# Kernel tuning notes

Hardware: AMD Instinct MI355X
Metric: run time of the kernel (lower is better)

The kernel has to match this reference:

```python
import jax, jax.numpy as jnp
import numpy as np

D_MODEL = 1024
NUM_HEADS = 16
SEG = 512            # segment_size
DIL = 4              # dilation_rate
HEAD_DIM = D_MODEL // NUM_HEADS


def setup_inputs() -> dict:
    key = jax.random.key(0)
    ks = jax.random.split(key, 5)
    B, S = 4, 4096
    sc = D_MODEL ** -0.5  # keep projected activations O(1) so softmax is not saturated
    def w(k):
        return jax.random.normal(k, (D_MODEL, D_MODEL), jnp.float32) * sc
    z = jnp.zeros((D_MODEL,), jnp.float32)
    return {
        "x": jax.random.normal(ks[0], (B, S, D_MODEL), jnp.float32),
        "Wq": w(ks[1]), "bq": z,
        "Wk": w(ks[2]), "bk": z,
        "Wv": w(ks[3]), "bv": z,
        "Wo": w(ks[4]), "bo": z,
    }


def reference(x, Wq, bq, Wk, bk, Wv, bv, Wo, bo):
    B, S, D = x.shape
    H, hd, seg, r = NUM_HEADS, HEAD_DIM, SEG, DIL
    scaling = hd ** -0.5

    Q = x @ Wq + bq
    K = x @ Wk + bk
    V = x @ Wv + bv

    pad = (-S) % seg
    if pad:
        Q = jnp.pad(Q, ((0, 0), (0, pad), (0, 0)))
        K = jnp.pad(K, ((0, 0), (0, pad), (0, 0)))
        V = jnp.pad(V, ((0, 0), (0, pad), (0, 0)))
    n = (S + pad) // seg          # num_segments
    sd = seg // r                 # dilated positions per segment per head

    # [B, n, sd, r, H, hd]: position within segment = t*r + offset
    def split(t):
        return t.reshape(B, n, sd, r, H, hd)

    offs = jnp.arange(H) % r      # per-head dilation offset sj = j % r
    hidx = jnp.arange(H)
    # vectorized per-head dilated gather -> [B, n, sd, H, hd]
    Qs = split(Q)[:, :, :, offs, hidx, :]
    Ks = split(K)[:, :, :, offs, hidx, :]
    Vs = split(V)[:, :, :, offs, hidx, :]

    # diagonal q.k score per dilated position, softmax over the segment's dilated positions
    scores = jnp.einsum('bnshd,bnshd->bnsh', Qs, Ks) * scaling
    probs = jax.nn.softmax(scores, axis=2)
    attn = probs[..., None] * Vs  # [B, n, sd, H, hd]

    # scatter back to each head's dilated positions; other positions stay zero
    out = jnp.zeros((B, n, sd, r, H, hd), x.dtype)
    out = out.at[:, :, :, offs, hidx, :].set(attn)
    out = out.reshape(B, n * seg, D)[:, :S]
    return out @ Wo + bo
```

## Files before the change

kernel.cpp:

```cpp
#include <hip/hip_runtime.h>
#include <hip/hip_bf16.h>

typedef unsigned short u16;
typedef unsigned int u32;
typedef __attribute__((ext_vector_type(8))) __bf16 bf16x8;
typedef __attribute__((ext_vector_type(4))) float f32x4;

#define NB 4
#define SQ 4096
#define DM 1024
#define RPC 4096
#define S4 (4 * DM)

#define VMCNT(n) asm volatile("s_waitcnt vmcnt(" #n ")" ::: "memory")
#define LGKM0()  asm volatile("s_waitcnt lgkmcnt(0)" ::: "memory")
#define BARRIER() asm volatile("s_barrier" ::: "memory")

__device__ __forceinline__ u16 f2b(float f) {
  u32 u = __builtin_bit_cast(u32, f);
  u32 r = u + 0x7fffu + ((u >> 16) & 1u);
  return (u16)(r >> 16);
}
__device__ __forceinline__ u32 cvt2(float lo, float hi) {
  u16 a = __builtin_bit_cast(u16, __float2bfloat16(lo));
  u16 b = __builtin_bit_cast(u16, __float2bfloat16(hi));
  return (u32)a | ((u32)b << 16);
}
__device__ __forceinline__ float dot2(u32 q, u32 k) {
  float ql = __builtin_bit_cast(float, q << 16);
  float qh = __builtin_bit_cast(float, q & 0xffff0000u);
  float kl = __builtin_bit_cast(float, k << 16);
  float kh = __builtin_bit_cast(float, k & 0xffff0000u);
  return ql * kl + qh * kh;
}
__device__ __forceinline__ u32 mul2(u32 v, float p) {
  float lo = __builtin_bit_cast(float, v << 16) * p;
  float hi = __builtin_bit_cast(float, v & 0xffff0000u) * p;
  return (u32)f2b(lo) | ((u32)f2b(hi) << 16);
}
__device__ __forceinline__ void gll16(const void* g, void* l) {
  __builtin_amdgcn_global_load_lds(
      (const __attribute__((address_space(1))) void*)g,
      (__attribute__((address_space(3))) void*)l, 16, 0, 0);
}

__global__ __launch_bounds__(256) void trans_qkv(const float* __restrict__ Wq,
                                                 const float* __restrict__ Wk,
                                                 const float* __restrict__ Wv,
                                                 u16* __restrict__ WTp) {
  __shared__ float T[64][65];
  const int k0 = blockIdx.x * 64, j0 = blockIdx.y * 64, c = blockIdx.z;
  const int msel = j0 >> 8;
  const float* W = (msel == 0) ? Wq : ((msel == 1) ? Wk : Wv);
  const int slot = (j0 & 255) >> 6;
  const int colbase = (c + 4 * slot) * 64;
  const int tid = threadIdx.x;
  const int rr = tid >> 6, cc = tid & 63;
#pragma unroll
  for (int it = 0; it < 16; ++it) {
    const int kk = rr + it * 4;
    T[kk][cc] = W[(size_t)(k0 + kk) * 1024 + colbase + cc];
  }
  __syncthreads();
  const int k64 = k0 >> 6;
  const int u = cc >> 3, e = cc & 7;
#pragma unroll
  for (int it = 0; it < 16; ++it) {
    const int jj = rr + it * 4;
    const int j = j0 + jj;
    const int n0 = j / 192, nrow = j - n0 * 192;
    WTp[((size_t)((c * 4 + n0) * 16 + k64)) * 12288 + nrow * 64 + (((u ^ (nrow & 7))) << 3) + e] =
        f2b(T[cc][jj]);
  }
}

__global__ __launch_bounds__(256) void trans_wo(const float* __restrict__ Wo,
                                                u16* __restrict__ WoTp) {
  __shared__ float T[64][65];
  const int j0 = blockIdx.x * 64, e0 = blockIdx.y * 64, c = blockIdx.z;
  const int rowbase = c * 64 + (j0 >> 6) * 256;
  const int tid = threadIdx.x;
  const int rr = tid >> 6, cc = tid & 63;
#pragma unroll
  for (int it = 0; it < 16; ++it) {
    const int jj = rr + it * 4;
    T[jj][cc] = Wo[(size_t)(rowbase + jj) * 1024 + e0 + cc];
  }
  __syncthreads();
  const int k64 = j0 >> 6;
  const int u = cc >> 3, e = cc & 7;
#pragma unroll
  for (int it = 0; it < 16; ++it) {
    const int ee = rr + it * 4;
    const int n = e0 + ee;
    const int n0 = n >> 8, nrow = n & 255;
    WoTp[((size_t)((c * 4 + n0) * 4 + k64)) * 16384 + nrow * 64 + (((u ^ (nrow & 7))) << 3) + e] =
        f2b(T[cc][ee]);
  }
}

__global__ __launch_bounds__(256) void bias_pack(const float* __restrict__ bq,
                                                 const float* __restrict__ bk,
                                                 const float* __restrict__ bv,
                                                 float* __restrict__ biasp) {
  const int idx = blockIdx.x * 256 + threadIdx.x;
  if (idx >= 3072) return;
  const int c = idx / 768, j = idx % 768;
  const int msel = j >> 8, jj = j & 255;
  const int col = (c + 4 * (jj >> 6)) * 64 + (jj & 63);
  const float* bb = (msel == 0) ? bq : ((msel == 1) ? bk : bv);
  biasp[idx] = bb[col];
}

__global__ __launch_bounds__(512, 2) void gemm_qkv(const float* __restrict__ x,
                                                   const u16* __restrict__ WTp,
                                                   const float* __restrict__ biasp,
                                                   u16* __restrict__ QKV) {
  __shared__ __align__(16) u16 As[2][16384];
  __shared__ __align__(16) u16 Bs[2][12288];
  const int p = blockIdx.x;
  const int L = (p & 7) * 32 + (p >> 3);
  const int c = L >> 6, rem = L & 63;
  const int m0 = rem >> 2, n0 = rem & 3;
  const int tid = threadIdx.x;
  const int lane = tid & 63, w = tid >> 6;
  const int wm = w >> 1, wn = w & 1;
  const int l15 = lane & 15, l16 = lane >> 4;

  const int rbase = m0 * 256;
  const int b = rbase >> 10;
  const int sbase = ((rbase & 1023) << 2) + c;
  const float* xA = x + (size_t)(b * SQ + sbase) * DM;

  int awoff[4];
  const float* aptr[4];
#pragma unroll
  for (int j = 0; j < 4; ++j) {
    const int r = (tid >> 3) + 64 * j;
    awoff[j] = r * 64 + (((tid & 7) ^ (r & 7)) << 3);
    aptr[j] = xA + (size_t)r * S4 + (tid & 7) * 8;
  }
  const u16* Bsrc = WTp + (size_t)((c * 4 + n0) * 16) * 12288;

  f32x4 acc[4][6];
#pragma unroll
  for (int i = 0; i < 4; ++i)
#pragma unroll
    for (int j = 0; j < 6; ++j) acc[i][j] = (f32x4){0.f, 0.f, 0.f, 0.f};

  int aoff[2][4], boff[2][6];
#pragma unroll
  for (int kk = 0; kk < 2; ++kk) {
    const int unit = kk * 4 + l16;
#pragma unroll
    for (int mf = 0; mf < 4; ++mf) {
      const int r = wm * 64 + mf * 16 + l15;
      aoff[kk][mf] = r * 64 + ((unit ^ (r & 7)) << 3);
    }
#pragma unroll
    for (int nf = 0; nf < 6; ++nf) {
      const int r = wn * 96 + nf * 16 + l15;
      boff[kk][nf] = r * 64 + ((unit ^ (r & 7)) << 3);
    }
  }

  float4 av[8];

#define LOADA(kt)                                                          \
  {                                                                        \
    _Pragma("unroll") for (int j = 0; j < 4; ++j) {                        \
      const float* s = aptr[j] + (kt) * 64;                                \
      av[2 * j] = *reinterpret_cast<const float4*>(s);                     \
      av[2 * j + 1] = *reinterpret_cast<const float4*>(s + 4);             \
    }                                                                      \
  }
#define DSWRITE(buf)                                                       \
  {                                                                        \
    _Pragma("unroll") for (int j = 0; j < 4; ++j) {                        \
      uint4 pk;                                                            \
      pk.x = cvt2(av[2 * j].x, av[2 * j].y);                               \
      pk.y = cvt2(av[2 * j].z, av[2 * j].w);                               \
      pk.z = cvt2(av[2 * j + 1].x, av[2 * j + 1].y);                       \
      pk.w = cvt2(av[2 * j + 1].z, av[2 * j + 1].w);                       \
      *reinterpret_cast<uint4*>(&As[buf][awoff[j]]) = pk;                  \
    }                                                                      \
  }
#define ISSUE_B(kt, buf)                                                   \
  {                                                                        \
    _Pragma("unroll") for (int i = 0; i < 3; ++i)                          \
        gll16(Bsrc + (size_t)(kt) * 12288 + tid * 8 + i * 4096,            \
              (char*)&Bs[buf][0] + tid * 16 + i * 8192);                   \
  }

  LOADA(0);
  DSWRITE(0);
  LOADA(1);
  ISSUE_B(0, 0);
  ISSUE_B(1, 1);
  VMCNT(6);
  DSWRITE(1);
  LOADA(2);
  VMCNT(8);
  LGKM0();
  BARRIER();

#pragma unroll 1
  for (int t = 0; t < 16; ++t) {
    const u16* Ab = As[t & 1];
    const u16* Bb = Bs[t & 1];
#pragma unroll
    for (int kk = 0; kk < 2; ++kk) {
      bf16x8 af[4], bv[6];
#pragma unroll
      for (int mf = 0; mf < 4; ++mf) af[mf] = *reinterpret_cast<const bf16x8*>(Ab + aoff[kk][mf]);
#pragma unroll
      for (int nf = 0; nf < 6; ++nf) bv[nf] = *reinterpret_cast<const bf16x8*>(Bb + boff[kk][nf]);
      __builtin_amdgcn_s_setprio(1);
#pragma unroll
      for (int mf = 0; mf < 4; ++mf)
#pragma unroll
        for (int nf = 0; nf < 6; ++nf)
          acc[mf][nf] = __builtin_amdgcn_mfma_f32_16x16x32_bf16(af[mf], bv[nf], acc[mf][nf], 0, 0, 0);
      __builtin_amdgcn_s_setprio(0);
    }
    if (t == 15) break;
    BARRIER();
    if (t <= 13) {
      VMCNT(8);
      ISSUE_B(t + 2, t & 1);
      VMCNT(3);
      DSWRITE(t & 1);
      if (t <= 12) LOADA(t + 3);
    } else {
      VMCNT(0);
    }
    LGKM0();
    BARRIER();
  }

  u16* outc = QKV + (size_t)c * RPC * 768;
#pragma unroll
  for (int mf = 0; mf < 4; ++mf) {
#pragma unroll
    for (int nf = 0; nf < 6; ++nf) {
      const int gcol = n0 * 192 + wn * 96 + nf * 16 + l15;
      const float bias = biasp[c * 768 + gcol];
#pragma unroll
      for (int jj = 0; jj < 4; ++jj) {
        const int rowt = wm * 64 + mf * 16 + l16 * 4 + jj;
        outc[(size_t)(rbase + rowt) * 768 + gcol] = f2b(acc[mf][nf][jj] + bias);
      }
    }
  }
#undef LOADA
#undef DSWRITE
#undef ISSUE_B
}

__global__ __launch_bounds__(256) void attn_k(const u16* __restrict__ QKV,
                                              u16* __restrict__ attnYp) {
  __shared__ float sc[4][128];
  const int blk = blockIdx.x;
  const int c = blk >> 6, b = (blk >> 4) & 3, n = (blk >> 1) & 7, half = blk & 1;
  const int r0 = b * 1024 + n * 128;
  const int m0 = r0 >> 8;
  const int rb = r0 & 255;
  const u16* base = QKV + ((size_t)c * RPC + r0) * 768;
  const int tid = threadIdx.x;
#pragma unroll
  for (int it = 0; it < 2; ++it) {
    const int tt = tid + it * 256;
    const int t = tt & 127, slot = tt >> 7;
    const u16* q = base + (size_t)t * 768 + slot * 64;
    float s = 0.f;
#pragma unroll
    for (int dd = 0; dd < 8; ++dd) {
      uint4 qa = *reinterpret_cast<const uint4*>(q + dd * 8);
      uint4 ka = *reinterpret_cast<const uint4*>(q + 256 + dd * 8);
      s += dot2(qa.x, ka.x) + dot2(qa.y, ka.y) + dot2(qa.z, ka.z) + dot2(qa.w, ka.w);
    }
    sc[slot][t] = s * 0.125f;
  }
  __syncthreads();
  const int w = tid >> 6, lane = tid & 63;
  float v0 = sc[w][lane], v1 = sc[w][lane + 64];
  float m = fmaxf(v0, v1);
#pragma unroll
  for (int off = 32; off; off >>= 1) m = fmaxf(m, __shfl_xor(m, off));
  float e0 = __expf(v0 - m), e1 = __expf(v1 - m);
  float ssum = e0 + e1;
#pragma unroll
  for (int off = 32; off; off >>= 1) ssum += __shfl_xor(ssum, off);
  const float inv = 1.f / ssum;
  sc[w][lane] = e0 * inv;
  sc[w][lane + 64] = e1 * inv;
  __syncthreads();
  u16* yout = attnYp + (size_t)((c * 16 + m0) * 4) * 16384;
#pragma unroll
  for (int it = 0; it < 8; ++it) {
    const int vi = tid + it * 256;
    const int t = vi >> 4, c8 = (vi & 15) + half * 16;
    const float pr = sc[c8 >> 3][t];
    uint4 va = *reinterpret_cast<const uint4*>(base + (size_t)t * 768 + 512 + c8 * 8);
    uint4 ra;
    ra.x = mul2(va.x, pr); ra.y = mul2(va.y, pr); ra.z = mul2(va.z, pr); ra.w = mul2(va.w, pr);
    const int rloc = rb + t;
    const int k64 = c8 >> 3, uu = c8 & 7, pp = uu ^ (rloc & 7);
    *reinterpret_cast<uint4*>(yout + k64 * 16384 + rloc * 64 + pp * 8) = ra;
  }
}

__global__ __launch_bounds__(512, 2) void gemm_out(const u16* __restrict__ attnYp,
                                                   const u16* __restrict__ WoTp,
                                                   const float* __restrict__ bo,
                                                   float* __restrict__ out) {
  __shared__ __align__(16) u16 As[2][16384];
  __shared__ __align__(16) u16 Bs[2][16384];
  const int p = blockIdx.x;
  const int L = (p & 7) * 32 + (p >> 3);
  const int c = L >> 6, rem = L & 63;
  const int m0 = rem >> 2, n0 = rem & 3;
  const int tid = threadIdx.x;
  const int lane = tid & 63, w = tid >> 6;
  const int wm = w >> 1, wn = w & 1;
  const int l15 = lane & 15, l16 = lane >> 4;

  const u16* Asrc = attnYp + (size_t)((c * 16 + m0) * 4) * 16384;
  const u16* Bsrc = WoTp + (size_t)((c * 4 + n0) * 4) * 16384;

  f32x4 acc[4][8];
#pragma unroll
  for (int i = 0; i < 4; ++i)
#pragma unroll
    for (int j = 0; j < 8; ++j) acc[i][j] = (f32x4){0.f, 0.f, 0.f, 0.f};

  int aoff[2][4], boff[2][8];
#pragma unroll
  for (int kk = 0; kk < 2; ++kk) {
    const int unit = kk * 4 + l16;
#pragma unroll
    for (int mf = 0; mf < 4; ++mf) {
      const int r = wm * 64 + mf * 16 + l15;
      aoff[kk][mf] = r * 64 + ((unit ^ (r & 7)) << 3);
    }
#pragma unroll
    for (int nf = 0; nf < 8; ++nf) {
      const int r = wn * 128 + nf * 16 + l15;
      boff[kk][nf] = r * 64 + ((unit ^ (r & 7)) << 3);
    }
  }

#define ISSUE(kt, buf)                                                     \
  {                                                                        \
    _Pragma("unroll") for (int i = 0; i < 4; ++i) {                        \
      gll16(Asrc + (size_t)(kt) * 16384 + tid * 8 + i * 4096,              \
            (char*)&As[buf][0] + tid * 16 + i * 8192);                     \
      gll16(Bsrc + (size_t)(kt) * 16384 + tid * 8 + i * 4096,              \
            (char*)&Bs[buf][0] + tid * 16 + i * 8192);                     \
    }                                                                      \
  }

  ISSUE(0, 0);
  ISSUE(1, 1);
  VMCNT(8);
  BARRIER();

#pragma unroll 1
  for (int t = 0; t < 4; ++t) {
    const u16* Ab = As[t & 1];
    const u16* Bb = Bs[t & 1];
#pragma unroll
    for (int kk = 0; kk < 2; ++kk) {
      bf16x8 af[4], bv[8];
#pragma unroll
      for (int mf = 0; mf < 4; ++mf) af[mf] = *reinterpret_cast<const bf16x8*>(Ab + aoff[kk][mf]);
#pragma unroll
      for (int nf = 0; nf < 8; ++nf) bv[nf] = *reinterpret_cast<const bf16x8*>(Bb + boff[kk][nf]);
      __builtin_amdgcn_s_setprio(1);
#pragma unroll
      for (int mf = 0; mf < 4; ++mf)
#pragma unroll
        for (int nf = 0; nf < 8; ++nf)
          acc[mf][nf] = __builtin_amdgcn_mfma_f32_16x16x32_bf16(af[mf], bv[nf], acc[mf][nf], 0, 0, 0);
      __builtin_amdgcn_s_setprio(0);
    }
    if (t == 3) break;
    BARRIER();
    if (t <= 1) {
      ISSUE(t + 2, t & 1);
      VMCNT(8);
    } else {
      VMCNT(0);
    }
    BARRIER();
  }
#undef ISSUE

  const int rbase = m0 * 256;
  const int b = rbase >> 10;
  const int sbase = ((rbase & 1023) << 2) + c;
  float* outp = out + (size_t)(b * SQ + sbase) * DM;
#pragma unroll
  for (int mf = 0; mf < 4; ++mf) {
#pragma unroll
    for (int nf = 0; nf < 8; ++nf) {
      const int gcol = n0 * 256 + wn * 128 + nf * 16 + l15;
      const float bias = bo[gcol];
#pragma unroll
      for (int jj = 0; jj < 4; ++jj) {
        const int rowt = wm * 64 + mf * 16 + l16 * 4 + jj;
        outp[(size_t)rowt * S4 + gcol] = acc[mf][nf][jj] + bias;
      }
    }
  }
}

extern "C" void kernel_launch(void* const* d_in, const int* in_sizes, int n_in,
                              void* d_out, int out_size, void* d_ws, size_t ws_size,
                              hipStream_t stream) {
  const float* x  = (const float*)d_in[0];
  const float* Wq = (const float*)d_in[1];
  const float* bq = (const float*)d_in[2];
  const float* Wk = (const float*)d_in[3];
  const float* bk = (const float*)d_in[4];
  const float* Wv = (const float*)d_in[5];
  const float* bv = (const float*)d_in[6];
  const float* Wo = (const float*)d_in[7];
  const float* bo = (const float*)d_in[8];
  float* out = (float*)d_out;

  char* ws = (char*)d_ws;
  u16*   WTp   = (u16*)(ws);
  float* biasp = (float*)(ws + 6291456);
  u16*   WoTp  = (u16*)(ws + 6303744);
  u16*   QKV   = (u16*)(ws + 8400896);
  u16*   attnYp= (u16*)(ws + 33566720);

  trans_qkv<<<dim3(16, 12, 4), 256, 0, stream>>>(Wq, Wk, Wv, WTp);
  bias_pack<<<12, 256, 0, stream>>>(bq, bk, bv, biasp);
  trans_wo<<<dim3(4, 16, 4), 256, 0, stream>>>(Wo, WoTp);
  gemm_qkv<<<256, 512, 0, stream>>>(x, WTp, biasp, QKV);
  attn_k<<<256, 256, 0, stream>>>(QKV, attnYp);
  gemm_out<<<256, 512, 0, stream>>>(attnYp, WoTp, bo, out);
}
```

Before: 84.05 us.

## Triple-buffer B tiles and overlap A staging with MFMA in QKV GEMM

Restructures the QKV GEMM main loop into a two-step unrolled pipeline. B tiles now rotate through three LDS buffers, and A uses two register sets. A fragments are read into registers before a barrier, which lets the next A global load, the B async copy and the LDS write of the following A tile be interleaved with the MFMA clusters. This removes one barrier per iteration and the serialized wait between compute and staging. In exchange it uses more LDS (an extra B buffer) and more registers, which may reduce occupancy under the 2-blocks launch bound.

Result: slower. 129.8 us (+54.5%).

```diff
diff --git a/kernel.cpp b/kernel.cpp
--- a/kernel.cpp
+++ b/kernel.cpp
@@ -116,8 +116,8 @@
                                                    const u16* __restrict__ WTp,
                                                    const float* __restrict__ biasp,
                                                    u16* __restrict__ QKV) {
-  __shared__ __align__(16) u16 As[2][16384];
-  __shared__ __align__(16) u16 Bs[2][12288];
+  __shared__ __align__(16) u16 As2[2 * 16384];
+  __shared__ __align__(16) u16 Bs3[3 * 12288];
   const int p = blockIdx.x;
   const int L = (p & 7) * 32 + (p >> 3);
   const int c = L >> 6, rem = L & 63;
@@ -132,14 +132,8 @@
   const int sbase = ((rbase & 1023) << 2) + c;
   const float* xA = x + (size_t)(b * SQ + sbase) * DM;
 
-  int awoff[4];
-  const float* aptr[4];
-#pragma unroll
-  for (int j = 0; j < 4; ++j) {
-    const int r = (tid >> 3) + 64 * j;
-    awoff[j] = r * 64 + (((tid & 7) ^ (r & 7)) << 3);
-    aptr[j] = xA + (size_t)r * S4 + (tid & 7) * 8;
-  }
+  const int aw0 = ((tid >> 3) * 64) + ((((tid & 7) ^ ((tid >> 3) & 7))) << 3);
+  const float* aptr = xA + (size_t)(tid >> 3) * S4 + (tid & 7) * 8;
   const u16* Bsrc = WTp + (size_t)((c * 4 + n0) * 16) * 12288;
 
   f32x4 acc[4][6];
@@ -148,94 +142,111 @@
 #pragma unroll
     for (int j = 0; j < 6; ++j) acc[i][j] = (f32x4){0.f, 0.f, 0.f, 0.f};
 
-  int aoff[2][4], boff[2][6];
+  int abase[2], bbase[2];
 #pragma unroll
   for (int kk = 0; kk < 2; ++kk) {
     const int unit = kk * 4 + l16;
-#pragma unroll
-    for (int mf = 0; mf < 4; ++mf) {
-      const int r = wm * 64 + mf * 16 + l15;
-      aoff[kk][mf] = r * 64 + ((unit ^ (r & 7)) << 3);
-    }
-#pragma unroll
-    for (int nf = 0; nf < 6; ++nf) {
-      const int r = wn * 96 + nf * 16 + l15;
-      boff[kk][nf] = r * 64 + ((unit ^ (r & 7)) << 3);
-    }
-  }
-
-  float4 av[8];
-
-#define LOADA(kt)                                                          \
+    abase[kk] = (wm * 64 + l15) * 64 + ((unit ^ (l15 & 7)) << 3);
+    bbase[kk] = (wn * 96 + l15) * 64 + ((unit ^ (l15 & 7)) << 3);
+  }
+
+  float4 av0[8], av1[8];
+
+#define LOADA(kt, AV)                                                      \
   {                                                                        \
     _Pragma("unroll") for (int j = 0; j < 4; ++j) {                        \
-      const float* s = aptr[j] + (kt) * 64;                                \
-      av[2 * j] = *reinterpret_cast<const float4*>(s);                     \
-      av[2 * j + 1] = *reinterpret_cast<const float4*>(s + 4);             \
+      const float* s = aptr + (size_t)j * (64 * S4) + (kt) * 64;           \
+      AV[2 * j] = *reinterpret_cast<const float4*>(s);                     \
+      AV[2 * j + 1] = *reinterpret_cast<const float4*>(s + 4);             \
     }                                                                      \
   }
-#define DSWRITE(buf)                                                       \
+#define DSWRITE(AV, bufLit)                                                \
   {                                                                        \
     _Pragma("unroll") for (int j = 0; j < 4; ++j) {                        \
       uint4 pk;                                                            \
-      pk.x = cvt2(av[2 * j].x, av[2 * j].y);                               \
-      pk.y = cvt2(av[2 * j].z, av[2 * j].w);                               \
-      pk.z = cvt2(av[2 * j + 1].x, av[2 * j + 1].y);                       \
-      pk.w = cvt2(av[2 * j + 1].z, av[2 * j + 1].w);                       \
-      *reinterpret_cast<uint4*>(&As[buf][awoff[j]]) = pk;                  \
+      pk.x = cvt2(AV[2 * j].x, AV[2 * j].y);                               \
+      pk.y = cvt2(AV[2 * j].z, AV[2 * j].w);                               \
+      pk.z = cvt2(AV[2 * j + 1].x, AV[2 * j + 1].y);                       \
+      pk.w = cvt2(AV[2 * j + 1].z, AV[2 * j + 1].w);                       \
+      *reinterpret_cast<uint4*>(&As2[(bufLit) * 16384 + aw0 + j * 4096]) = pk; \
     }                                                                      \
   }
-#define ISSUE_B(kt, buf)                                                   \
-  {                                                                        \
+#define ISSUE_B(kt)                                                        \
+  {                                                                        \
+    const int dst3 = (kt) % 3;                                             \
     _Pragma("unroll") for (int i = 0; i < 3; ++i)                          \
         gll16(Bsrc + (size_t)(kt) * 12288 + tid * 8 + i * 4096,            \
-              (char*)&Bs[buf][0] + tid * 16 + i * 8192);                   \
-  }
-
-  LOADA(0);
-  DSWRITE(0);
-  LOADA(1);
-  ISSUE_B(0, 0);
-  ISSUE_B(1, 1);
-  VMCNT(6);
-  DSWRITE(1);
-  LOADA(2);
+              (char*)Bs3 + dst3 * 24576 + tid * 16 + i * 8192);            \
+  }
+#define READ_A(Ab, AF0, AF1)                                               \
+  {                                                                        \
+    _Pragma("unroll") for (int mf = 0; mf < 4; ++mf) {                     \
+      AF0[mf] = *reinterpret_cast<const bf16x8*>((Ab) + abase[0] + mf * 1024); \
+      AF1[mf] = *reinterpret_cast<const bf16x8*>((Ab) + abase[1] + mf * 1024); \
+    }                                                                      \
+  }
+#define MFMA_CL(AF, kk)                                                    \
+  {                                                                        \
+    bf16x8 bv[6];                                                          \
+    _Pragma("unroll") for (int nf = 0; nf < 6; ++nf)                       \
+        bv[nf] = *reinterpret_cast<const bf16x8*>(Bb + bbase[kk] + nf * 1024); \
+    __builtin_amdgcn_s_setprio(1);                                         \
+    _Pragma("unroll") for (int mf = 0; mf < 4; ++mf)                       \
+        _Pragma("unroll") for (int nf = 0; nf < 6; ++nf)                   \
+            acc[mf][nf] = __builtin_amdgcn_mfma_f32_16x16x32_bf16(          \
+                AF[mf], bv[nf], acc[mf][nf], 0, 0, 0);                     \
+    __builtin_amdgcn_s_setprio(0);                                         \
+  }
+
+  LOADA(0, av0);
+  LOADA(1, av1);
+  ISSUE_B(0);
+  ISSUE_B(1);
+  DSWRITE(av0, 0);
+  DSWRITE(av1, 1);
+  LOADA(2, av0);
   VMCNT(8);
   LGKM0();
   BARRIER();
 
 #pragma unroll 1
-  for (int t = 0; t < 16; ++t) {
-    const u16* Ab = As[t & 1];
-    const u16* Bb = Bs[t & 1];
-#pragma unroll
-    for (int kk = 0; kk < 2; ++kk) {
-      bf16x8 af[4], bv[6];
-#pragma unroll
-      for (int mf = 0; mf < 4; ++mf) af[mf] = *reinterpret_cast<const bf16x8*>(Ab + aoff[kk][mf]);
-#pragma unroll
-      for (int nf = 0; nf < 6; ++nf) bv[nf] = *reinterpret_cast<const bf16x8*>(Bb + boff[kk][nf]);
-      __builtin_amdgcn_s_setprio(1);
-#pragma unroll
-      for (int mf = 0; mf < 4; ++mf)
-#pragma unroll
-        for (int nf = 0; nf < 6; ++nf)
-          acc[mf][nf] = __builtin_amdgcn_mfma_f32_16x16x32_bf16(af[mf], bv[nf], acc[mf][nf], 0, 0, 0);
-      __builtin_amdgcn_s_setprio(0);
-    }
-    if (t == 15) break;
-    BARRIER();
-    if (t <= 13) {
-      VMCNT(8);
-      ISSUE_B(t + 2, t & 1);
-      VMCNT(3);
-      DSWRITE(t & 1);
-      if (t <= 12) LOADA(t + 3);
-    } else {
-      VMCNT(0);
-    }
-    LGKM0();
-    BARRIER();
+  for (int tp = 0; tp < 8; ++tp) {
+    {
+      const int t = 2 * tp;
+      const u16* Ab = As2;
+      const u16* Bb = Bs3 + (t % 3) * 12288;
+      bf16x8 af0[4], af1[4];
+      READ_A(Ab, af0, af1);
+      LGKM0();
+      BARRIER();
+      if (t <= 12) LOADA(t + 3, av1);
+      if (t <= 13) ISSUE_B(t + 2);
+      MFMA_CL(af0, 0);
+      if (t <= 13) DSWRITE(av0, 0);
+      MFMA_CL(af1, 1);
+      LGKM0();
+      if (t < 14) { VMCNT(11); } else { VMCNT(0); }
+      BARRIER();
+    }
+    {
+      const int t = 2 * tp + 1;
+      const u16* Ab = As2 + 16384;
+      const u16* Bb = Bs3 + (t % 3) * 12288;
+      bf16x8 af0[4], af1[4];
+      READ_A(Ab, af0, af1);
+      LGKM0();
+      BARRIER();
+      if (t <= 12) LOADA(t + 3, av0);
+      if (t <= 13) ISSUE_B(t + 2);
+      MFMA_CL(af0, 0);
+      if (t <= 13) DSWRITE(av1, 1);
+      MFMA_CL(af1, 1);
+      if (t < 15) {
+        LGKM0();
+        VMCNT(11);
+        BARRIER();
+      }
+    }
   }
 
   u16* outc = QKV + (size_t)c * RPC * 768;
@@ -255,6 +266,8 @@
 #undef LOADA
 #undef DSWRITE
 #undef ISSUE_B
+#undef READ_A
+#undef MFMA_CL
 }
 
 __global__ __launch_bounds__(256) void attn_k(const u16* __restrict__ QKV,
```

## Pre-pack x to swizzled bf16 and stream A via direct-to-LDS loads

Applied to the files above, without the earlier changes.

A new pack_x kernel converts the fp32 input to bf16 once, in the dilated, swizzled tile layout. gemm_qkv can then load A tiles with global_load_lds into a triple-buffered LDS ring instead of doing register loads, conversion and LDS writes inside the main loop. Launch bounds drop to one block per SM, and some intermediates move into the output buffer to fit workspace. This removes the in-loop conversion and register staging, at the cost of an extra kernel launch and a full read and write of x in bf16.

After: 102.9 us. +22.4%, slower.

```diff
diff --git a/kernel.cpp b/kernel.cpp
--- a/kernel.cpp
+++ b/kernel.cpp
@@ -13,7 +13,6 @@
 #define S4 (4 * DM)
 
 #define VMCNT(n) asm volatile("s_waitcnt vmcnt(" #n ")" ::: "memory")
-#define LGKM0()  asm volatile("s_waitcnt lgkmcnt(0)" ::: "memory")
 #define BARRIER() asm volatile("s_barrier" ::: "memory")
 
 __device__ __forceinline__ u16 f2b(float f) {
@@ -42,6 +41,38 @@
   __builtin_amdgcn_global_load_lds(
       (const __attribute__((address_space(1))) void*)g,
       (__attribute__((address_space(3))) void*)l, 16, 0, 0);
+}
+
+__global__ __launch_bounds__(256) void pack_x(const float* __restrict__ x,
+                                              u16* __restrict__ xbT) {
+  const int k64 = blockIdx.x;
+  const int m0 = blockIdx.y;
+  const int c = blockIdx.z;
+  const int tid = threadIdx.x;
+  const int b = m0 >> 2;
+  const int s0 = (m0 & 3) * 256;
+  const int rt = tid >> 2;
+  const int q4 = tid & 3;
+  u16* dst = xbT + ((size_t)((c * 16 + m0) * 16 + k64)) * 16384;
+  const float* src =
+      x + ((size_t)(b * SQ + (s0 + rt) * 4 + c)) * DM + k64 * 64 + q4 * 16;
+#pragma unroll
+  for (int j = 0; j < 4; ++j) {
+    const int r = rt + j * 64;
+    const float* s = src + (size_t)j * 64 * S4;
+    float4 v0 = *reinterpret_cast<const float4*>(s);
+    float4 v1 = *reinterpret_cast<const float4*>(s + 4);
+    float4 v2 = *reinterpret_cast<const float4*>(s + 8);
+    float4 v3 = *reinterpret_cast<const float4*>(s + 12);
+    uint4 pk0, pk1;
+    pk0.x = cvt2(v0.x, v0.y); pk0.y = cvt2(v0.z, v0.w);
+    pk0.z = cvt2(v1.x, v1.y); pk0.w = cvt2(v1.z, v1.w);
+    pk1.x = cvt2(v2.x, v2.y); pk1.y = cvt2(v2.z, v2.w);
+    pk1.z = cvt2(v3.x, v3.y); pk1.w = cvt2(v3.z, v3.w);
+    const int u0 = q4 * 2;
+    *reinterpret_cast<uint4*>(dst + r * 64 + ((u0 ^ (r & 7)) << 3)) = pk0;
+    *reinterpret_cast<uint4*>(dst + r * 64 + (((u0 + 1) ^ (r & 7)) << 3)) = pk1;
+  }
 }
 
 __global__ __launch_bounds__(256) void trans_qkv(const float* __restrict__ Wq,
@@ -112,12 +143,12 @@
   biasp[idx] = bb[col];
 }
 
-__global__ __launch_bounds__(512, 2) void gemm_qkv(const float* __restrict__ x,
+__global__ __launch_bounds__(512, 1) void gemm_qkv(const u16* __restrict__ xbT,
                                                    const u16* __restrict__ WTp,
                                                    const float* __restrict__ biasp,
                                                    u16* __restrict__ QKV) {
-  __shared__ __align__(16) u16 As[2][16384];
-  __shared__ __align__(16) u16 Bs[2][12288];
+  __shared__ __align__(16) u16 As3[3 * 16384];
+  __shared__ __align__(16) u16 Bs2[2 * 12288];
   const int p = blockIdx.x;
   const int L = (p & 7) * 32 + (p >> 3);
   const int c = L >> 6, rem = L & 63;
@@ -127,19 +158,7 @@
   const int wm = w >> 1, wn = w & 1;
   const int l15 = lane & 15, l16 = lane >> 4;
 
-  const int rbase = m0 * 256;
-  const int b = rbase >> 10;
-  const int sbase = ((rbase & 1023) << 2) + c;
-  const float* xA = x + (size_t)(b * SQ + sbase) * DM;
-
-  int awoff[4];
-  const float* aptr[4];
-#pragma unroll
-  for (int j = 0; j < 4; ++j) {
-    const int r = (tid >> 3) + 64 * j;
-    awoff[j] = r * 64 + (((tid & 7) ^ (r & 7)) << 3);
-    aptr[j] = xA + (size_t)r * S4 + (tid & 7) * 8;
-  }
+  const u16* Asrc = xbT + (size_t)((c * 16 + m0) * 16) * 16384;
   const u16* Bsrc = WTp + (size_t)((c * 4 + n0) * 16) * 12288;
 
   f32x4 acc[4][6];
@@ -148,73 +167,49 @@
 #pragma unroll
     for (int j = 0; j < 6; ++j) acc[i][j] = (f32x4){0.f, 0.f, 0.f, 0.f};
 
-  int aoff[2][4], boff[2][6];
+  int abase[2], bbase[2];
 #pragma unroll
   for (int kk = 0; kk < 2; ++kk) {
     const int unit = kk * 4 + l16;
-#pragma unroll
-    for (int mf = 0; mf < 4; ++mf) {
-      const int r = wm * 64 + mf * 16 + l15;
-      aoff[kk][mf] = r * 64 + ((unit ^ (r & 7)) << 3);
-    }
-#pragma unroll
-    for (int nf = 0; nf < 6; ++nf) {
-      const int r = wn * 96 + nf * 16 + l15;
-      boff[kk][nf] = r * 64 + ((unit ^ (r & 7)) << 3);
-    }
-  }
-
-  float4 av[8];
-
-#define LOADA(kt)                                                          \
+    abase[kk] = (wm * 64 + l15) * 64 + ((unit ^ (l15 & 7)) << 3);
+    bbase[kk] = (wn * 96 + l15) * 64 + ((unit ^ (l15 & 7)) << 3);
+  }
+
+#define ISSUE_A(kt, buf)                                                   \
   {                                                                        \
-    _Pragma("unroll") for (int j = 0; j < 4; ++j) {                        \
-      const float* s = aptr[j] + (kt) * 64;                                \
-      av[2 * j] = *reinterpret_cast<const float4*>(s);                     \
-      av[2 * j + 1] = *reinterpret_cast<const float4*>(s + 4);             \
-    }                                                                      \
-  }
-#define DSWRITE(buf)                                                       \
-  {                                                                        \
-    _Pragma("unroll") for (int j = 0; j < 4; ++j) {                        \
-      uint4 pk;                                                            \
-      pk.x = cvt2(av[2 * j].x, av[2 * j].y);                               \
-      pk.y = cvt2(av[2 * j].z, av[2 * j].w);                               \
-      pk.z = cvt2(av[2 * j + 1].x, av[2 * j + 1].y);                       \
-      pk.w = cvt2(av[2 * j + 1].z, av[2 * j + 1].w);                       \
-      *reinterpret_cast<uint4*>(&As[buf][awoff[j]]) = pk;                  \
-    }                                                                      \
+    _Pragma("unroll") for (int i = 0; i < 4; ++i)                          \
+        gll16(Asrc + (size_t)(kt) * 16384 + tid * 8 + i * 4096,            \
+              (char*)As3 + (buf) * 32768 + tid * 16 + i * 8192);           \
   }
 #define ISSUE_B(kt, buf)                                                   \
   {                                                                        \
     _Pragma("unroll") for (int i = 0; i < 3; ++i)                          \
         gll16(Bsrc + (size_t)(kt) * 12288 + tid * 8 + i * 4096,            \
-              (char*)&Bs[buf][0] + tid * 16 + i * 8192);                   \
-  }
-
-  LOADA(0);
-  DSWRITE(0);
-  LOADA(1);
+              (char*)Bs2 + (buf) * 24576 + tid * 16 + i * 8192);           \
+  }
+
+  ISSUE_A(0, 0);
   ISSUE_B(0, 0);
+  ISSUE_A(1, 1);
   ISSUE_B(1, 1);
-  VMCNT(6);
-  DSWRITE(1);
-  LOADA(2);
-  VMCNT(8);
-  LGKM0();
+  ISSUE_A(2, 2);
+  VMCNT(11);
   BARRIER();
 
+  int abuf = 0, bbuf = 0;
 #pragma unroll 1
   for (int t = 0; t < 16; ++t) {
-    const u16* Ab = As[t & 1];
-    const u16* Bb = Bs[t & 1];
+    const u16* Ab = As3 + abuf * 16384;
+    const u16* Bb = Bs2 + bbuf * 12288;
 #pragma unroll
     for (int kk = 0; kk < 2; ++kk) {
       bf16x8 af[4], bv[6];
 #pragma unroll
-      for (int mf = 0; mf < 4; ++mf) af[mf] = *reinterpret_cast<const bf16x8*>(Ab + aoff[kk][mf]);
-#pragma unroll
-      for (int nf = 0; nf < 6; ++nf) bv[nf] = *reinterpret_cast<const bf16x8*>(Bb + boff[kk][nf]);
+      for (int mf = 0; mf < 4; ++mf)
+        af[mf] = *reinterpret_cast<const bf16x8*>(Ab + abase[kk] + mf * 1024);
+#pragma unroll
+      for (int nf = 0; nf < 6; ++nf)
+        bv[nf] = *reinterpret_cast<const bf16x8*>(Bb + bbase[kk] + nf * 1024);
       __builtin_amdgcn_s_setprio(1);
 #pragma unroll
       for (int mf = 0; mf < 4; ++mf)
@@ -225,19 +220,19 @@
     }
     if (t == 15) break;
     BARRIER();
-    if (t <= 13) {
-      VMCNT(8);
-      ISSUE_B(t + 2, t & 1);
-      VMCNT(3);
-      DSWRITE(t & 1);
-      if (t <= 12) LOADA(t + 3);
-    } else {
-      VMCNT(0);
-    }
-    LGKM0();
+    if (t <= 12) ISSUE_A(t + 3, abuf);
+    if (t <= 13) ISSUE_B(t + 2, bbuf);
+    if (t <= 12) { VMCNT(7); }
+    else if (t == 13) { VMCNT(3); }
+    else { VMCNT(0); }
     BARRIER();
-  }
-
+    abuf = (abuf == 2) ? 0 : abuf + 1;
+    bbuf ^= 1;
+  }
+#undef ISSUE_A
+#undef ISSUE_B
+
+  const int rbase = m0 * 256;
   u16* outc = QKV + (size_t)c * RPC * 768;
 #pragma unroll
   for (int mf = 0; mf < 4; ++mf) {
@@ -252,9 +247,6 @@
       }
     }
   }
-#undef LOADA
-#undef DSWRITE
-#undef ISSUE_B
 }
 
 __global__ __launch_bounds__(256) void attn_k(const u16* __restrict__ QKV,
@@ -310,7 +302,7 @@
   }
 }
 
-__global__ __launch_bounds__(512, 2) void gemm_out(const u16* __restrict__ attnYp,
+__global__ __launch_bounds__(512, 1) void gemm_out(const u16* __restrict__ attnYp,
                                                    const u16* __restrict__ WoTp,
                                                    const float* __restrict__ bo,
                                                    float* __restrict__ out) {
@@ -430,16 +422,20 @@
   float* out = (float*)d_out;
 
   char* ws = (char*)d_ws;
-  u16*   WTp   = (u16*)(ws);
-  float* biasp = (float*)(ws + 6291456);
-  u16*   WoTp  = (u16*)(ws + 6303744);
-  u16*   QKV   = (u16*)(ws + 8400896);
-  u16*   attnYp= (u16*)(ws + 33566720);
-
+  u16* xbT    = (u16*)(ws);
+  u16* WoTp   = (u16*)(ws + 33554432);
+  u16* attnYp = (u16*)(ws + 35651584);
+
+  char* ob = (char*)d_out;
+  u16*   QKV   = (u16*)(ob);
+  u16*   WTp   = (u16*)(ob + 33554432);
+  float* biasp = (float*)(ob + 39845888);
+
+  pack_x<<<dim3(16, 16, 4), 256, 0, stream>>>(x, xbT);
   trans_qkv<<<dim3(16, 12, 4), 256, 0, stream>>>(Wq, Wk, Wv, WTp);
   bias_pack<<<12, 256, 0, stream>>>(bq, bk, bv, biasp);
   trans_wo<<<dim3(4, 16, 4), 256, 0, stream>>>(Wo, WoTp);
-  gemm_qkv<<<256, 512, 0, stream>>>(x, WTp, biasp, QKV);
+  gemm_qkv<<<256, 512, 0, stream>>>(xbT, WTp, biasp, QKV);
   attn_k<<<256, 256, 0, stream>>>(QKV, attnYp);
   gemm_out<<<256, 512, 0, stream>>>(attnYp, WoTp, bo, out);
 }
```
